# Kernel optimization log

Measured on AMD Instinct MI355X. Metric: run time of the kernel, lower is better.

## Reference

```python
import jax, jax.numpy as jnp
import numpy as np

DIM = 512
HEADS = 8
HD = DIM // HEADS
HIDDEN = 4 * DIM
EPS = 1e-5


def layernorm(x, g, b):
    mu = jnp.mean(x, axis=-1, keepdims=True)
    var = jnp.mean(jnp.square(x - mu), axis=-1, keepdims=True)
    return (x - mu) * jax.lax.rsqrt(var + EPS) * g + b


def setup_inputs() -> dict:
    key = jax.random.key(0)
    ks = jax.random.split(key, 10)
    B, P, N, C = 16, 4, 256, DIM
    s = 1.0 / np.sqrt(C)
    sh = 1.0 / np.sqrt(HIDDEN)
    return {
        "x": jax.random.normal(ks[0], (B, P, N, C), jnp.float32),
        "ln1_g": jnp.ones((C,), jnp.float32),
        "ln1_b": jnp.zeros((C,), jnp.float32),
        "w_qkv": jax.random.uniform(ks[1], (3 * C, C), jnp.float32, -s, s),
        "w_proj": jax.random.uniform(ks[2], (C, C), jnp.float32, -s, s),
        "b_proj": jax.random.uniform(ks[3], (C,), jnp.float32, -s, s),
        "ln2_g": jnp.ones((C,), jnp.float32),
        "ln2_b": jnp.zeros((C,), jnp.float32),
        "w1": jax.random.uniform(ks[4], (HIDDEN, C), jnp.float32, -s, s),
        "b1": jax.random.uniform(ks[5], (HIDDEN,), jnp.float32, -s, s),
        "w2": jax.random.uniform(ks[6], (C, HIDDEN), jnp.float32, -sh, sh),
        "b2": jax.random.uniform(ks[7], (C,), jnp.float32, -sh, sh),
    }


def reference(x, ln1_g, ln1_b, w_qkv, w_proj, b_proj, ln2_g, ln2_b, w1, b1, w2, b2):
    B, P, N, C = x.shape
    # --- attention branch (batched over B, P, heads; same math as the unrolled loops) ---
    h = layernorm(x, ln1_g, ln1_b)
    qkv = jnp.einsum('bpnc,dc->bpnd', h, w_qkv)            # [B,P,N,3C]
    qkv = qkv.reshape(B, P, N, 3, HEADS, HD)
    q, k, v = qkv[..., 0, :, :], qkv[..., 1, :, :], qkv[..., 2, :, :]  # [B,P,N,H,hd]
    scale = HD ** -0.5
    attn = jnp.einsum('bpnhd,bpmhd->bphnm', q * scale, k)  # [B,P,H,N,N]
    attn = jax.nn.softmax(attn, axis=-1)
    o = jnp.einsum('bphnm,bpmhd->bpnhd', attn, v).reshape(B, P, N, C)
    o = jnp.einsum('bpnc,dc->bpnd', o, w_proj) + b_proj
    x = x + o
    # --- MLP branch ---
    h = layernorm(x, ln2_g, ln2_b)
    h = jax.nn.gelu(jnp.einsum('bpnc,hc->bpnh', h, w1) + b1, approximate=False)
    h = jnp.einsum('bpnh,ch->bpnc', h, w2) + b2
    return x + h
```

## Files before the change

### kernel.cpp

```cpp
#include <hip/hip_runtime.h>

typedef __attribute__((ext_vector_type(8))) short short8;
typedef __attribute__((ext_vector_type(4))) float f32x4;

__device__ __forceinline__ float bf2f(unsigned short u) {
    return __uint_as_float(((unsigned)u) << 16);
}
__device__ __forceinline__ unsigned short f2bf(float f) {
    unsigned u = __float_as_uint(f);
    u += 0x7fffu + ((u >> 16) & 1u);
    return (unsigned short)(u >> 16);
}
__device__ __forceinline__ void load_lds16(const void* g, void* l) {
    __builtin_amdgcn_global_load_lds(
        (const __attribute__((address_space(1))) void*)g,
        (__attribute__((address_space(3))) void*)l, 16, 0, 0);
}
__device__ __forceinline__ bool is_bf16(const unsigned* dt) {
    return *dt == 0x3F803F80u;
}
__device__ __forceinline__ float gelu_fast(float t) {
    float u = t * (0.7978845608f + 0.0356774081f * t * t);
    float e = __expf(-2.0f * fabsf(u));
    float th = (1.0f - e) / (1.0f + e);
    th = copysignf(th, u);
    return 0.5f * t * (1.0f + th);
}

__global__ __launch_bounds__(512) void cast_all(
    const void* s_wqkv, const void* s_wproj, const void* s_w1, const void* s_w2,
    const void* v0, const void* v1, const void* v2, const void* v3,
    const void* v4, const void* v5, const void* v6,
    unsigned short* d_wqkv, unsigned short* d_wproj, unsigned short* d_w1,
    unsigned short* d_w2, unsigned short* par, const unsigned* dt)
{
    bool isbf = is_bf16(dt);
    int b = blockIdx.x, tid = threadIdx.x;
    if (b < 768) {
        const void* src; unsigned short* dst; int off;
        if (b < 192)      { src = s_wqkv;  dst = d_wqkv;  off = b * 4096; }
        else if (b < 256) { src = s_wproj; dst = d_wproj; off = (b - 192) * 4096; }
        else if (b < 512) { src = s_w1;    dst = d_w1;    off = (b - 256) * 4096; }
        else              { src = s_w2;    dst = d_w2;    off = (b - 512) * 4096; }
        int i = off + tid * 8;
        if (isbf) {
            *(short8*)(dst + i) = *(const short8*)((const unsigned short*)src + i);
        } else {
            const float* s = (const float*)src + i;
            short8 o;
            #pragma unroll
            for (int j = 0; j < 8; ++j) o[j] = (short)f2bf(s[j]);
            *(short8*)(dst + i) = o;
        }
    } else {
        const void* srcs[7]  = {v0, v1, v2, v3, v4, v5, v6};
        const int   sizes[7] = {512, 512, 512, 512, 512, 2048, 512};
        const int   offs[7]  = {0, 512, 1024, 1536, 2048, 2560, 4608};
        int j = b - 768;
        const void* s = srcs[j];
        unsigned short* d = par + offs[j];
        for (int i = tid; i < sizes[j]; i += 512)
            d[i] = isbf ? ((const unsigned short*)s)[i] : f2bf(((const float*)s)[i]);
    }
}

__global__ __launch_bounds__(256) void ln_kernel(
    const void* __restrict__ xin, size_t row0,
    const unsigned* __restrict__ dt, int force_f32,
    const unsigned short* __restrict__ g, const unsigned short* __restrict__ b,
    unsigned short* __restrict__ y)
{
    int w = threadIdx.x >> 6, lane = threadIdx.x & 63;
    size_t lr = (size_t)blockIdx.x * 4 + w;
    size_t gr = row0 + lr;
    bool isf32 = force_f32 || !is_bf16(dt);
    float v[8];
    if (isf32) {
        const float* xr = (const float*)xin + (gr << 9) + (lane << 3);
        #pragma unroll
        for (int j = 0; j < 8; ++j) v[j] = xr[j];
    } else {
        short8 raw = *(const short8*)((const unsigned short*)xin + (gr << 9) + (lane << 3));
        #pragma unroll
        for (int j = 0; j < 8; ++j) v[j] = bf2f((unsigned short)raw[j]);
    }
    float sum = 0.f, sq = 0.f;
    #pragma unroll
    for (int j = 0; j < 8; ++j) { sum += v[j]; sq += v[j] * v[j]; }
    #pragma unroll
    for (int off = 32; off > 0; off >>= 1) {
        sum += __shfl_xor(sum, off);
        sq  += __shfl_xor(sq, off);
    }
    float mu  = sum * (1.0f / 512.0f);
    float var = sq * (1.0f / 512.0f) - mu * mu;
    float rs  = rsqrtf(var + 1e-5f);
    short8 gr8 = *(const short8*)(g + (lane << 3));
    short8 br8 = *(const short8*)(b + (lane << 3));
    short8 outv;
    #pragma unroll
    for (int j = 0; j < 8; ++j) {
        float o = (v[j] - mu) * rs * bf2f((unsigned short)gr8[j]) + bf2f((unsigned short)br8[j]);
        outv[j] = (short)f2bf(o);
    }
    *(short8*)(y + (lr << 9) + (lane << 3)) = outv;
}

template<int BN>
__global__ __launch_bounds__(256) void gemm4(
    const unsigned short* __restrict__ A, const unsigned short* __restrict__ W,
    const unsigned short* __restrict__ bias,
    const void* __restrict__ resid, size_t rrow0,
    void* __restrict__ out, size_t orow0,
    int NBY, int N, int K, int mode, const unsigned* __restrict__ dt)
{
    constexpr int MI = (BN == 128) ? 4 : 2;
    constexpr int BROUNDS = BN / 64;
    constexpr int BUFB = 8192 + BN * 64;
    __shared__ char lds[2][BUFB];
    int tid = threadIdx.x;
    int w = tid >> 6, lane = tid & 63;
    int l15 = lane & 15, g = lane >> 4;

    int L = blockIdx.x;
    int bx, by;
    if ((NBY & 7) == 0) {
        int nby8 = NBY >> 3;
        int xcd = L & 7, i = L >> 3;
        by = xcd * nby8 + (i % nby8);
        bx = i / nby8;
    } else {
        by = L % NBY;
        bx = L / NBY;
    }
    int m0 = by << 7, n0 = bx * BN;
    int wm = (BN == 128) ? ((w >> 1) << 6) : (w << 5);
    int wn = (BN == 128) ? ((w & 1) << 6) : 0;

    int srow_t = ((tid >> 3) << 1) | (tid & 1);
    int u_t = ((tid >> 1) & 3) ^ ((tid >> 3) & 3);
    const unsigned short* gA[2];
    const unsigned short* gB[BROUNDS];
    #pragma unroll
    for (int j = 0; j < 2; ++j)
        gA[j] = A + (size_t)(m0 + j * 64 + srow_t) * K + u_t * 8;
    #pragma unroll
    for (int j = 0; j < BROUNDS; ++j)
        gB[j] = W + (size_t)(n0 + j * 64 + srow_t) * K + u_t * 8;
    int lslot = tid * 16;

    int off = (l15 >> 1) * 128 + ((g ^ ((l15 >> 1) & 3)) << 5) + ((l15 & 1) << 4);

    f32x4 acc[MI][4];
    #pragma unroll
    for (int i = 0; i < MI; ++i)
        #pragma unroll
        for (int j = 0; j < 4; ++j) acc[i][j] = (f32x4){0.f, 0.f, 0.f, 0.f};

    #pragma unroll
    for (int j = 0; j < 2; ++j)
        load_lds16(gA[j], &lds[0][j * 4096 + lslot]);
    #pragma unroll
    for (int j = 0; j < BROUNDS; ++j)
        load_lds16(gB[j], &lds[0][8192 + j * 4096 + lslot]);

    int p = 0;
    for (int k = 0; k < K; k += 32) {
        __syncthreads();
        if (k + 32 < K) {
            int kn = k + 32;
            #pragma unroll
            for (int j = 0; j < 2; ++j)
                load_lds16(gA[j] + kn, &lds[p ^ 1][j * 4096 + lslot]);
            #pragma unroll
            for (int j = 0; j < BROUNDS; ++j)
                load_lds16(gB[j] + kn, &lds[p ^ 1][8192 + j * 4096 + lslot]);
        }
        const char* bA = &lds[p][0];
        const char* bB = &lds[p][8192];
        short8 af[MI], bfr[4];
        #pragma unroll
        for (int i = 0; i < MI; ++i)
            af[i] = *(const short8*)(bA + (wm + i * 16) * 64 + off);
        #pragma unroll
        for (int j = 0; j < 4; ++j)
            bfr[j] = *(const short8*)(bB + (wn + j * 16) * 64 + off);
        #pragma unroll
        for (int i = 0; i < MI; ++i)
            #pragma unroll
            for (int j = 0; j < 4; ++j)
                acc[i][j] = __builtin_amdgcn_mfma_f32_16x16x32_bf16(af[i], bfr[j], acc[i][j], 0, 0, 0);
        p ^= 1;
    }

    char* tb = (char*)lds;
    __syncthreads();
    #pragma unroll
    for (int j = 0; j < 4; ++j) {
        int colL = wn + j * 16 + l15;
        int ccb = colL >> 3, cb = (colL & 7) << 1;
        #pragma unroll
        for (int i = 0; i < MI; ++i) {
            #pragma unroll
            for (int r = 0; r < 4; ++r) {
                int row = wm + i * 16 + g * 4 + r;
                *(unsigned short*)(tb + row * (BN * 2) + ((ccb ^ (row & 7)) << 4) + cb)
                    = f2bf(acc[i][j][r]);
            }
        }
    }
    __syncthreads();

    constexpr int CHR = BN / 8;
    constexpr int RPP = 256 / CHR;
    constexpr int NPASS = 128 / RPP;
    int rL = tid / CHR;
    int lc = tid % CHR;
    bool inbf = is_bf16(dt);
    int colg = n0 + lc * 8;
    float bv[8];
    if (bias) {
        short8 bb = *(const short8*)(bias + colg);
        #pragma unroll
        for (int t = 0; t < 8; ++t) bv[t] = bf2f((unsigned short)bb[t]);
    } else {
        #pragma unroll
        for (int t = 0; t < 8; ++t) bv[t] = 0.f;
    }

    for (int ps = 0; ps < NPASS; ++ps) {
        int row = ps * RPP + rL;
        int rowL = m0 + row;
        short8 vv = *(const short8*)(tb + row * (BN * 2) + ((lc ^ (row & 7)) << 4));
        float vals[8];
        #pragma unroll
        for (int t = 0; t < 8; ++t) vals[t] = bf2f((unsigned short)vv[t]) + bv[t];

        if (mode == 0) {
            *(short8*)((unsigned short*)out + (size_t)rowL * N + colg) = vv;
        } else if (mode == 2) {
            short8 ov;
            #pragma unroll
            for (int t = 0; t < 8; ++t) ov[t] = (short)f2bf(gelu_fast(vals[t]));
            *(short8*)((unsigned short*)out + (size_t)rowL * N + colg) = ov;
        } else if (mode == 1) {
            size_t rbase = (rrow0 + rowL) * (size_t)N + colg;
            float o8[8];
            if (inbf) {
                short8 rr = *(const short8*)((const unsigned short*)resid + rbase);
                #pragma unroll
                for (int t = 0; t < 8; ++t) o8[t] = bf2f((unsigned short)rr[t]) + vals[t];
            } else {
                f32x4 r0 = *(const f32x4*)((const float*)resid + rbase);
                f32x4 r1 = *(const f32x4*)((const float*)resid + rbase + 4);
                #pragma unroll
                for (int t = 0; t < 4; ++t) { o8[t] = r0[t] + vals[t]; o8[t + 4] = r1[t] + vals[t + 4]; }
            }
            float* ob = (float*)out + (size_t)rowL * N + colg;
            *(f32x4*)ob       = (f32x4){o8[0], o8[1], o8[2], o8[3]};
            *(f32x4*)(ob + 4) = (f32x4){o8[4], o8[5], o8[6], o8[7]};
        } else {
            size_t rbase = (size_t)rowL * N + colg;
            f32x4 r0 = *(const f32x4*)((const float*)resid + rbase);
            f32x4 r1 = *(const f32x4*)((const float*)resid + rbase + 4);
            float o8[8];
            #pragma unroll
            for (int t = 0; t < 4; ++t) { o8[t] = r0[t] + vals[t]; o8[t + 4] = r1[t] + vals[t + 4]; }
            size_t obase = (orow0 + rowL) * (size_t)N + colg;
            if (inbf) {
                short8 ov;
                #pragma unroll
                for (int t = 0; t < 8; ++t) ov[t] = (short)f2bf(o8[t]);
                *(short8*)((unsigned short*)out + obase) = ov;
            } else {
                float* ob = (float*)out + obase;
                *(f32x4*)ob       = (f32x4){o8[0], o8[1], o8[2], o8[3]};
                *(f32x4*)(ob + 4) = (f32x4){o8[4], o8[5], o8[6], o8[7]};
            }
        }
    }
}

__global__ __launch_bounds__(256) void attn_mfma(
    const unsigned short* __restrict__ qkv, unsigned short* __restrict__ o)
{
    __shared__ unsigned short Vt[64 * 256];
    __shared__ unsigned short Ps[4][16 * 256];
    int bp = blockIdx.x >> 3, h = blockIdx.x & 7;
    const unsigned short* base = qkv + (size_t)bp * 256 * 1536;
    int qo = h << 6, ko = 512 + (h << 6), vo = 1024 + (h << 6);
    int tid = threadIdx.x, w = tid >> 6, lane = tid & 63;
    int l15 = lane & 15, g = lane >> 4;

    {
        int d = tid & 63;
        for (int s = tid >> 6; s < 256; s += 4) {
            unsigned short v = base[(size_t)s * 1536 + vo + d];
            *(unsigned short*)((char*)Vt + d * 512 + (((s >> 3) ^ (d & 7)) << 4) + ((s & 7) << 1)) = v;
        }
    }
    __syncthreads();

    unsigned short* P = Ps[w];

    for (int pass = 0; pass < 4; ++pass) {
        int q0 = pass * 64 + w * 16;
        short8 qa[2];
        #pragma unroll
        for (int t = 0; t < 2; ++t)
            qa[t] = *(const short8*)(base + (size_t)(q0 + l15) * 1536 + qo + t * 32 + g * 8);
        f32x4 S[16];
        #pragma unroll
        for (int ns = 0; ns < 16; ++ns) {
            f32x4 a = {0.f, 0.f, 0.f, 0.f};
            #pragma unroll
            for (int t = 0; t < 2; ++t) {
                short8 kb = *(const short8*)(base + (size_t)(ns * 16 + l15) * 1536 + ko + t * 32 + g * 8);
                a = __builtin_amdgcn_mfma_f32_16x16x32_bf16(qa[t], kb, a, 0, 0, 0);
            }
            S[ns] = a;
        }
        float mx[4], sums[4], inv[4];
        #pragma unroll
        for (int r = 0; r < 4; ++r) {
            float m = -1e30f;
            #pragma unroll
            for (int ns = 0; ns < 16; ++ns) m = fmaxf(m, S[ns][r]);
            m *= 0.125f;
            #pragma unroll
            for (int off = 1; off < 16; off <<= 1) m = fmaxf(m, __shfl_xor(m, off));
            mx[r] = m;
            sums[r] = 0.f;
        }
        #pragma unroll
        for (int ns = 0; ns < 16; ++ns)
            #pragma unroll
            for (int r = 0; r < 4; ++r) {
                float p = __expf(S[ns][r] * 0.125f - mx[r]);
                sums[r] += p;
                S[ns][r] = p;
            }
        #pragma unroll
        for (int r = 0; r < 4; ++r) {
            float s2 = sums[r];
            #pragma unroll
            for (int off = 1; off < 16; off <<= 1) s2 += __shfl_xor(s2, off);
            inv[r] = 1.0f / s2;
        }
        #pragma unroll
        for (int ns = 0; ns < 16; ++ns)
            #pragma unroll
            for (int r = 0; r < 4; ++r) {
                int mq = g * 4 + r;
                int s = ns * 16 + l15;
                *(unsigned short*)((char*)P + mq * 512 + (((s >> 3) ^ (mq & 7)) << 4) + ((s & 7) << 1))
                    = f2bf(S[ns][r] * inv[r]);
            }
        f32x4 O[4];
        #pragma unroll
        for (int ds = 0; ds < 4; ++ds) O[ds] = (f32x4){0.f, 0.f, 0.f, 0.f};
        #pragma unroll
        for (int ks = 0; ks < 8; ++ks) {
            int c = (ks * 4 + g) ^ (l15 & 7);
            short8 pa = *(const short8*)((const char*)P + l15 * 512 + (c << 4));
            #pragma unroll
            for (int ds = 0; ds < 4; ++ds) {
                short8 vb = *(const short8*)((const char*)Vt + (ds * 16 + l15) * 512 + (c << 4));
                O[ds] = __builtin_amdgcn_mfma_f32_16x16x32_bf16(pa, vb, O[ds], 0, 0, 0);
            }
        }
        #pragma unroll
        for (int ds = 0; ds < 4; ++ds)
            #pragma unroll
            for (int r = 0; r < 4; ++r) {
                int mq = q0 + g * 4 + r;
                int d = ds * 16 + l15;
                o[((size_t)(bp * 256 + mq) << 9) + (h << 6) + d] = f2bf(O[ds][r]);
            }
    }
}

extern "C" void kernel_launch(void* const* d_in, const int* in_sizes, int n_in,
                              void* d_out, int out_size, void* d_ws, size_t ws_size,
                              hipStream_t stream)
{
    const void* x      = d_in[0];
    const void* ln1_g  = d_in[1];
    const void* ln1_b  = d_in[2];
    const void* w_qkv  = d_in[3];
    const void* w_proj = d_in[4];
    const void* b_proj = d_in[5];
    const void* ln2_g  = d_in[6];
    const void* ln2_b  = d_in[7];
    const void* w1     = d_in[8];
    const void* b1     = d_in[9];
    const void* w2     = d_in[10];
    const void* b2     = d_in[11];
    const unsigned* dt = (const unsigned*)ln1_g;

    const int M = 16384;
    char* ws = (char*)d_ws;
    unsigned short* wqkv_b  = (unsigned short*)(ws);
    unsigned short* wproj_b = (unsigned short*)(ws + 1572864);
    unsigned short* w1_b    = (unsigned short*)(ws + 2097152);
    unsigned short* w2_b    = (unsigned short*)(ws + 4194304);
    unsigned short* par     = (unsigned short*)(ws + 6291456);
    const size_t CAST_END = 6308096;

    unsigned short* p_g1    = par + 0;
    unsigned short* p_b1ln  = par + 512;
    unsigned short* p_bproj = par + 1024;
    unsigned short* p_g2    = par + 1536;
    unsigned short* p_b2ln  = par + 2048;
    unsigned short* p_b1    = par + 2560;
    unsigned short* p_b2    = par + 4608;

    int NC = 64;
    const int cand[7] = {1, 2, 4, 8, 16, 32, 64};
    for (int i = 0; i < 7; ++i) {
        size_t need = CAST_END + (size_t)(M / cand[i]) * 11264;
        if (need <= ws_size) { NC = cand[i]; break; }
    }
    const int R = M / NC;
    const int NBY = R / 128;

    char* cb = ws + CAST_END;
    unsigned short* h   = (unsigned short*)(cb);
    unsigned short* qkv = (unsigned short*)(cb + (size_t)R * 1024);
    unsigned short* o   = (unsigned short*)(cb + (size_t)R * 4096);
    float*          x2  = (float*)        (cb + (size_t)R * 5120);
    unsigned short* hid = (unsigned short*)(cb + (size_t)R * 7168);
    unsigned short* h2  = h;

    cast_all<<<775, 512, 0, stream>>>(w_qkv, w_proj, w1, w2,
                                      ln1_g, ln1_b, b_proj, ln2_g, ln2_b, b1, b2,
                                      wqkv_b, wproj_b, w1_b, w2_b, par, dt);

    for (int c = 0; c < NC; ++c) {
        const size_t r0 = (size_t)c * R;

        ln_kernel<<<R / 4, 256, 0, stream>>>(x, r0, dt, 0, p_g1, p_b1ln, h);
        gemm4<128><<<(1536 / 128) * NBY, 256, 0, stream>>>(
            h, wqkv_b, nullptr, nullptr, 0, qkv, 0, NBY, 1536, 512, 0, dt);
        attn_mfma<<<(R / 256) * 8, 256, 0, stream>>>(qkv, o);
        gemm4<64><<<(512 / 64) * NBY, 256, 0, stream>>>(
            o, wproj_b, p_bproj, x, r0, x2, 0, NBY, 512, 512, 1, dt);
        ln_kernel<<<R / 4, 256, 0, stream>>>(x2, 0, dt, 1, p_g2, p_b2ln, h2);
        gemm4<128><<<(2048 / 128) * NBY, 256, 0, stream>>>(
            h2, w1_b, p_b1, nullptr, 0, hid, 0, NBY, 2048, 512, 2, dt);
        gemm4<64><<<(512 / 64) * NBY, 256, 0, stream>>>(
            hid, w2_b, p_b2, x2, 0, d_out, r0, NBY, 512, 2048, 3, dt);
    }
}
```

Measured before the change: 353.3 us.

## Replace GEMM tiles with unified 256x128 block tile for all projections

New measurement: 347.8 us. Within noise of the previous version (-1.6%).

```diff
diff --git a/kernel.cpp b/kernel.cpp
--- a/kernel.cpp
+++ b/kernel.cpp
@@ -106,18 +106,18 @@
     *(short8*)(y + (lr << 9) + (lane << 3)) = outv;
 }
 
-template<int BN>
-__global__ __launch_bounds__(256) void gemm4(
+__global__ __launch_bounds__(256, 2) void gemm5(
     const unsigned short* __restrict__ A, const unsigned short* __restrict__ W,
     const unsigned short* __restrict__ bias,
     const void* __restrict__ resid, size_t rrow0,
     void* __restrict__ out, size_t orow0,
     int NBY, int N, int K, int mode, const unsigned* __restrict__ dt)
 {
-    constexpr int MI = (BN == 128) ? 4 : 2;
-    constexpr int BROUNDS = BN / 64;
-    constexpr int BUFB = 8192 + BN * 64;
-    __shared__ char lds[2][BUFB];
+    constexpr int BM = 256, BN = 128;
+    constexpr int MI = 8;
+    constexpr int BUFB = (BM + BN) * 64;
+    __shared__ char lds[BM * BN * 2];
+
     int tid = threadIdx.x;
     int w = tid >> 6, lane = tid & 63;
     int l15 = lane & 15, g = lane >> 4;
@@ -133,19 +133,19 @@
         by = L % NBY;
         bx = L / NBY;
     }
-    int m0 = by << 7, n0 = bx * BN;
-    int wm = (BN == 128) ? ((w >> 1) << 6) : (w << 5);
-    int wn = (BN == 128) ? ((w & 1) << 6) : 0;
+    int m0 = by << 8, n0 = bx << 7;
+    int wm = (w >> 1) << 7;
+    int wn = (w & 1) << 6;
 
     int srow_t = ((tid >> 3) << 1) | (tid & 1);
     int u_t = ((tid >> 1) & 3) ^ ((tid >> 3) & 3);
-    const unsigned short* gA[2];
-    const unsigned short* gB[BROUNDS];
+    const unsigned short* gA[4];
+    const unsigned short* gB[2];
+    #pragma unroll
+    for (int j = 0; j < 4; ++j)
+        gA[j] = A + (size_t)(m0 + j * 64 + srow_t) * K + u_t * 8;
     #pragma unroll
     for (int j = 0; j < 2; ++j)
-        gA[j] = A + (size_t)(m0 + j * 64 + srow_t) * K + u_t * 8;
-    #pragma unroll
-    for (int j = 0; j < BROUNDS; ++j)
         gB[j] = W + (size_t)(n0 + j * 64 + srow_t) * K + u_t * 8;
     int lslot = tid * 16;
 
@@ -158,26 +158,27 @@
         for (int j = 0; j < 4; ++j) acc[i][j] = (f32x4){0.f, 0.f, 0.f, 0.f};
 
     #pragma unroll
+    for (int j = 0; j < 4; ++j)
+        load_lds16(gA[j], &lds[j * 4096 + lslot]);
+    #pragma unroll
     for (int j = 0; j < 2; ++j)
-        load_lds16(gA[j], &lds[0][j * 4096 + lslot]);
-    #pragma unroll
-    for (int j = 0; j < BROUNDS; ++j)
-        load_lds16(gB[j], &lds[0][8192 + j * 4096 + lslot]);
+        load_lds16(gB[j], &lds[16384 + j * 4096 + lslot]);
 
     int p = 0;
     for (int k = 0; k < K; k += 32) {
         __syncthreads();
         if (k + 32 < K) {
             int kn = k + 32;
+            char* nb = &lds[(p ^ 1) * BUFB];
+            #pragma unroll
+            for (int j = 0; j < 4; ++j)
+                load_lds16(gA[j] + kn, nb + j * 4096 + lslot);
             #pragma unroll
             for (int j = 0; j < 2; ++j)
-                load_lds16(gA[j] + kn, &lds[p ^ 1][j * 4096 + lslot]);
-            #pragma unroll
-            for (int j = 0; j < BROUNDS; ++j)
-                load_lds16(gB[j] + kn, &lds[p ^ 1][8192 + j * 4096 + lslot]);
-        }
-        const char* bA = &lds[p][0];
-        const char* bB = &lds[p][8192];
+                load_lds16(gB[j] + kn, nb + 16384 + j * 4096 + lslot);
+        }
+        const char* bA = &lds[p * BUFB];
+        const char* bB = bA + 16384;
         short8 af[MI], bfr[4];
         #pragma unroll
         for (int i = 0; i < MI; ++i)
@@ -204,18 +205,15 @@
             #pragma unroll
             for (int r = 0; r < 4; ++r) {
                 int row = wm + i * 16 + g * 4 + r;
-                *(unsigned short*)(tb + row * (BN * 2) + ((ccb ^ (row & 7)) << 4) + cb)
+                *(unsigned short*)(tb + row * 256 + ((ccb ^ (row & 15)) << 4) + cb)
                     = f2bf(acc[i][j][r]);
             }
         }
     }
     __syncthreads();
 
-    constexpr int CHR = BN / 8;
-    constexpr int RPP = 256 / CHR;
-    constexpr int NPASS = 128 / RPP;
-    int rL = tid / CHR;
-    int lc = tid % CHR;
+    int rL = tid >> 4;
+    int lc = tid & 15;
     bool inbf = is_bf16(dt);
     int colg = n0 + lc * 8;
     float bv[8];
@@ -228,10 +226,10 @@
         for (int t = 0; t < 8; ++t) bv[t] = 0.f;
     }
 
-    for (int ps = 0; ps < NPASS; ++ps) {
-        int row = ps * RPP + rL;
+    for (int ps = 0; ps < 16; ++ps) {
+        int row = ps * 16 + rL;
         int rowL = m0 + row;
-        short8 vv = *(const short8*)(tb + row * (BN * 2) + ((lc ^ (row & 7)) << 4));
+        short8 vv = *(const short8*)(tb + row * 256 + ((lc ^ (row & 15)) << 4));
         float vals[8];
         #pragma unroll
         for (int t = 0; t < 8; ++t) vals[t] = bf2f((unsigned short)vv[t]) + bv[t];
@@ -422,7 +420,7 @@
         if (need <= ws_size) { NC = cand[i]; break; }
     }
     const int R = M / NC;
-    const int NBY = R / 128;
+    const int NBY = R / 256;
 
     char* cb = ws + CAST_END;
     unsigned short* h   = (unsigned short*)(cb);
@@ -440,15 +438,15 @@
         const size_t r0 = (size_t)c * R;
 
         ln_kernel<<<R / 4, 256, 0, stream>>>(x, r0, dt, 0, p_g1, p_b1ln, h);
-        gemm4<128><<<(1536 / 128) * NBY, 256, 0, stream>>>(
+        gemm5<<<(1536 / 128) * NBY, 256, 0, stream>>>(
             h, wqkv_b, nullptr, nullptr, 0, qkv, 0, NBY, 1536, 512, 0, dt);
         attn_mfma<<<(R / 256) * 8, 256, 0, stream>>>(qkv, o);
-        gemm4<64><<<(512 / 64) * NBY, 256, 0, stream>>>(
+        gemm5<<<(512 / 128) * NBY, 256, 0, stream>>>(
             o, wproj_b, p_bproj, x, r0, x2, 0, NBY, 512, 512, 1, dt);
         ln_kernel<<<R / 4, 256, 0, stream>>>(x2, 0, dt, 1, p_g2, p_b2ln, h2);
-        gemm4<128><<<(2048 / 128) * NBY, 256, 0, stream>>>(
+        gemm5<<<(2048 / 128) * NBY, 256, 0, stream>>>(
             h2, w1_b, p_b1, nullptr, 0, hid, 0, NBY, 2048, 512, 2, dt);
-        gemm4<64><<<(512 / 64) * NBY, 256, 0, stream>>>(
+        gemm5<<<(512 / 128) * NBY, 256, 0, stream>>>(
             hid, w2_b, p_b2, x2, 0, d_out, r0, NBY, 512, 2048, 3, dt);
     }
 }
```
